# Optimization experiments

Measured on AMD Instinct MI355X. Metric: run time of the kernel, lower is better.

The kernel has to match this reference:

```python
import jax, jax.numpy as jnp
import numpy as np

SPARSE_COMPRESSION_RATIO = 0.5  # config.sparse_compression_ratio


def setup_inputs() -> dict:
    key = jax.random.key(0)
    kv_cache = jax.random.normal(key, (2, 32, 4096, 128), dtype=jnp.float32)
    return {"kv_cache": kv_cache}


def reference(kv_cache):
    # elements_to_keep = int(numel * (1 - ratio))
    total = kv_cache.size
    k = int(total * (1.0 - SPARSE_COMPRESSION_RATIO))
    flat = kv_cache.reshape(-1)
    # torch.topk(|x|, k, largest=True) -> indices of k largest magnitudes
    _, top_idx = jax.lax.top_k(jnp.abs(flat), k)
    # scatter mask, then elementwise multiply (zeros out non-top-k entries)
    mask = jnp.zeros((total,), dtype=jnp.bool_).at[top_idx].set(True)
    return kv_cache * mask.reshape(kv_cache.shape)
```

## Files before the change

kernel.cpp:

```cpp
#include <hip/hip_runtime.h>
#include <stdint.h>


#define NTHR 256
#define MASK31 0x7fffffffu

#define SH_OFF    0
#define SH_BINS   8192
#define CH_OFF    8192
#define CH_BINS   4096
#define SCL_OFF   12288
#define L3_OFF    12304
#define L3_CAP    4096
#define PAIRS_OFF (L3_OFF + 2 * L3_CAP)
#define PAIRS_CAP (1u << 20)
#define ZERO_WORDS (SCL_OFF + 16)

#define STG_CAP   2048

__global__ void zero_ws_kernel(uint32_t* __restrict__ ws) {
    int i = blockIdx.x * blockDim.x + threadIdx.x;
    if (i < ZERO_WORDS) ws[i] = 0;
}

__global__ void sample_hist_kernel(const uint4* __restrict__ xv, long long n4,
                                   uint32_t* __restrict__ ws) {
    __shared__ uint32_t lh[SH_BINS];
    for (int i = threadIdx.x; i < SH_BINS; i += NTHR) lh[i] = 0;
    __syncthreads();
    long long S4 = n4 >> 5;
    long long T = (long long)gridDim.x * NTHR;
    for (long long s = (long long)blockIdx.x * NTHR + threadIdx.x; s < S4; s += T) {
        long long g = s >> 6;
        long long idx4 = g * 2048 + ((g & 31) << 6) + (s & 63);
        uint4 v = xv[idx4];
        atomicAdd(&lh[(v.x & MASK31) >> 18], 1u);
        atomicAdd(&lh[(v.y & MASK31) >> 18], 1u);
        atomicAdd(&lh[(v.z & MASK31) >> 18], 1u);
        atomicAdd(&lh[(v.w & MASK31) >> 18], 1u);
    }
    __syncthreads();
    for (int i = threadIdx.x; i < SH_BINS; i += NTHR)
        if (lh[i]) atomicAdd(&ws[SH_OFF + i], lh[i]);
}

__global__ void sel_bracket_kernel(uint32_t* __restrict__ ws,
                                   uint32_t ksmM, uint32_t kspM) {
    __shared__ uint32_t lh[SH_BINS];
    __shared__ uint32_t csum[NTHR];
    __shared__ uint32_t cpre[NTHR];
    __shared__ int sBHi, sB1;
    for (int i = threadIdx.x; i < SH_BINS; i += NTHR) lh[i] = ws[SH_OFF + i];
    if (threadIdx.x == 0) { sBHi = -1; sB1 = -1; }
    __syncthreads();
    uint32_t s = 0;
    for (int i = 0; i < 32; ++i) s += lh[threadIdx.x * 32 + i];
    csum[threadIdx.x] = s;
    __syncthreads();
    if (threadIdx.x == 0) {
        uint32_t run = 0;
        for (int c = NTHR - 1; c >= 0; --c) { cpre[c] = run; run += csum[c]; }
    }
    __syncthreads();
    {
        int c = threadIdx.x;
        int hitHi = -1, hitB1 = -1;
        uint32_t excl = cpre[c];
        for (int bb = c * 32 + 31; bb >= c * 32; --bb) {
            uint32_t cnt = lh[bb];
            uint32_t incl = excl + cnt;
            if (hitHi < 0 && incl >= ksmM) hitHi = bb;
            if (hitB1 < 0 && excl >= kspM) hitB1 = bb;
            excl = incl;
        }
        if (hitHi >= 0) atomicMax(&sBHi, hitHi);
        if (hitB1 >= 0) atomicMax(&sB1, hitB1);
    }
    __syncthreads();
    if (threadIdx.x == 0) {
        int bHi = sBHi < 0 ? 0 : sBHi;
        int bLo = sB1 + 1;
        if (bLo > bHi) bLo = bHi;
        if (bLo < 0) bLo = 0;
        int sbins = bHi - bLo + 1;
        int clog = 0; while ((1 << clog) < sbins) ++clog;
        int spanBits = 18 + clog;
        int shift1 = spanBits - 12;
        if (shift1 < 0) shift1 = 0;
        ws[SCL_OFF + 0] = ((uint32_t)bLo) << 18;
        ws[SCL_OFF + 1] = ((uint32_t)(bHi + 1)) << 18;
        ws[SCL_OFF + 2] = (uint32_t)shift1;
    }
}

__global__ void fused_main_kernel(const uint32_t* __restrict__ x,
                                  uint32_t* __restrict__ out, long long n,
                                  uint32_t* __restrict__ ws) {
    __shared__ uint2 stage[STG_CAP];
    __shared__ uint32_t cnt, sBase, redHi[NTHR / 64];
    const uint32_t uLo = ws[SCL_OFF + 0];
    const uint32_t uHi = ws[SCL_OFF + 1];
    const uint32_t span = uHi - uLo;
    if (threadIdx.x == 0) cnt = 0u;
    __syncthreads();

    const uint4* __restrict__ xv = (const uint4*)x;
    uint4* __restrict__ ov = (uint4*)out;
    uint2* __restrict__ gpairs = (uint2*)(ws + PAIRS_OFF);
    long long n4 = n >> 2;
    const long long stride = (long long)gridDim.x * NTHR;
    const long long i0 = (long long)blockIdx.x * NTHR + threadIdx.x;

    uint32_t myHi = 0;
    uint32_t hitIter = 0;
    uint32_t it = 0;
    long long i = i0;
    for (; i + stride < n4; i += 2 * stride, it += 2) {
        uint4 va = xv[i];
        uint4 vb = xv[i + stride];
        uint32_t a0 = va.x & MASK31, a1 = va.y & MASK31;
        uint32_t a2 = va.z & MASK31, a3 = va.w & MASK31;
        uint32_t b0 = vb.x & MASK31, b1 = vb.y & MASK31;
        uint32_t b2 = vb.z & MASK31, b3 = vb.w & MASK31;
        myHi += (uint32_t)(a0 >= uHi) + (uint32_t)(a1 >= uHi)
              + (uint32_t)(a2 >= uHi) + (uint32_t)(a3 >= uHi)
              + (uint32_t)(b0 >= uHi) + (uint32_t)(b1 >= uHi)
              + (uint32_t)(b2 >= uHi) + (uint32_t)(b3 >= uHi);
        uint32_t ha = (uint32_t)((a0 - uLo) < span) | (uint32_t)((a1 - uLo) < span)
                    | (uint32_t)((a2 - uLo) < span) | (uint32_t)((a3 - uLo) < span);
        uint32_t hb = (uint32_t)((b0 - uLo) < span) | (uint32_t)((b1 - uLo) < span)
                    | (uint32_t)((b2 - uLo) < span) | (uint32_t)((b3 - uLo) < span);
        hitIter |= ha << (it & 31);
        hitIter |= hb << ((it + 1) & 31);
        uint4 oa, ob;
        oa.x = (a0 >= uHi) ? va.x : 0u;
        oa.y = (a1 >= uHi) ? va.y : 0u;
        oa.z = (a2 >= uHi) ? va.z : 0u;
        oa.w = (a3 >= uHi) ? va.w : 0u;
        ob.x = (b0 >= uHi) ? vb.x : 0u;
        ob.y = (b1 >= uHi) ? vb.y : 0u;
        ob.z = (b2 >= uHi) ? vb.z : 0u;
        ob.w = (b3 >= uHi) ? vb.w : 0u;
        ov[i] = oa;
        ov[i + stride] = ob;
    }
    if (i < n4) {
        uint4 v = xv[i];
        uint32_t a0 = v.x & MASK31, a1 = v.y & MASK31;
        uint32_t a2 = v.z & MASK31, a3 = v.w & MASK31;
        myHi += (uint32_t)(a0 >= uHi) + (uint32_t)(a1 >= uHi)
              + (uint32_t)(a2 >= uHi) + (uint32_t)(a3 >= uHi);
        uint32_t ha = (uint32_t)((a0 - uLo) < span) | (uint32_t)((a1 - uLo) < span)
                    | (uint32_t)((a2 - uLo) < span) | (uint32_t)((a3 - uLo) < span);
        hitIter |= ha << (it & 31);
        uint4 o;
        o.x = (a0 >= uHi) ? v.x : 0u;
        o.y = (a1 >= uHi) ? v.y : 0u;
        o.z = (a2 >= uHi) ? v.z : 0u;
        o.w = (a3 >= uHi) ? v.w : 0u;
        ov[i] = o;
    }

#define PUSHP(val, eidx) { \
    uint32_t p_ = atomicAdd(&cnt, 1u); \
    uint2 pr_ = make_uint2((val), (eidx)); \
    if (p_ < STG_CAP) stage[p_] = pr_; \
    else { uint32_t g_ = atomicAdd(&ws[SCL_OFF + 4], 1u); \
           if (g_ < PAIRS_CAP) gpairs[g_] = pr_; } }

    if (blockIdx.x == 0) {
        for (long long idx = (n4 << 2) + threadIdx.x; idx < n; idx += NTHR) {
            uint32_t v = x[idx];
            uint32_t u = v & MASK31;
            myHi += (uint32_t)(u >= uHi);
            if (u - uLo < span) PUSHP(v, (uint32_t)idx)
            out[idx] = (u >= uHi) ? v : 0u;
        }
    }

    while (hitIter) {
        uint32_t b = __ffs(hitIter) - 1u;
        hitIter &= hitIter - 1u;
        for (long long ii = i0 + (long long)b * stride; ii < n4; ii += (stride << 5)) {
            uint4 v = xv[ii];
            uint32_t e0 = (uint32_t)(ii << 2);
            uint32_t u;
            u = v.x & MASK31; if (u - uLo < span) PUSHP(v.x, e0 + 0u)
            u = v.y & MASK31; if (u - uLo < span) PUSHP(v.y, e0 + 1u)
            u = v.z & MASK31; if (u - uLo < span) PUSHP(v.z, e0 + 2u)
            u = v.w & MASK31; if (u - uLo < span) PUSHP(v.w, e0 + 3u)
        }
    }
#undef PUSHP

    for (int o = 32; o > 0; o >>= 1) myHi += __shfl_down(myHi, o);
    if ((threadIdx.x & 63) == 0) redHi[threadIdx.x >> 6] = myHi;
    __syncthreads();
    if (threadIdx.x == 0) {
        uint32_t tot = 0;
        for (int w = 0; w < NTHR / 64; ++w) tot += redHi[w];
        if (tot) atomicAdd(&ws[SCL_OFF + 3], tot);
        uint32_t c = cnt < STG_CAP ? cnt : STG_CAP;
        cnt = c;
        sBase = atomicAdd(&ws[SCL_OFF + 4], c);
    }
    __syncthreads();
    uint32_t c = cnt, bw = sBase;
    for (uint32_t q = threadIdx.x; q < c; q += NTHR)
        if (bw + q < PAIRS_CAP) gpairs[bw + q] = stage[q];
}

__global__ void cand_hist_kernel(uint32_t* __restrict__ ws) {
    __shared__ uint32_t lh[CH_BINS];
    uint32_t G = ws[SCL_OFF + 4]; if (G > PAIRS_CAP) G = PAIRS_CAP;
    uint32_t uLo = ws[SCL_OFF + 0], shift1 = ws[SCL_OFF + 2];
    for (int i = threadIdx.x; i < CH_BINS; i += NTHR) lh[i] = 0;
    __syncthreads();
    const uint2* pairs = (const uint2*)(ws + PAIRS_OFF);
    uint32_t stride = gridDim.x * NTHR;
    for (uint32_t i = blockIdx.x * NTHR + threadIdx.x; i < G; i += stride) {
        uint32_t u = pairs[i].x & MASK31;
        atomicAdd(&lh[((u - uLo) >> shift1) & (CH_BINS - 1)], 1u);
    }
    __syncthreads();
    for (int i = threadIdx.x; i < CH_BINS; i += NTHR)
        if (lh[i]) atomicAdd(&ws[CH_OFF + i], lh[i]);
}

__global__ void sel_gather_kernel(uint32_t* __restrict__ ws, uint32_t k) {
    __shared__ uint32_t lh[CH_BINS];
    __shared__ uint32_t csum[NTHR];
    __shared__ uint32_t cpre[NTHR];
    __shared__ uint32_t sBase2, sRem2, sKp;
    for (int i = threadIdx.x; i < CH_BINS; i += NTHR) lh[i] = ws[CH_OFF + i];
    __syncthreads();
    uint32_t s = 0;
    for (int i = 0; i < 16; ++i) s += lh[threadIdx.x * 16 + i];
    csum[threadIdx.x] = s;
    __syncthreads();
    if (threadIdx.x == 0) {
        uint32_t run = 0;
        for (int c = NTHR - 1; c >= 0; --c) { cpre[c] = run; run += csum[c]; }
        uint32_t cntHi = ws[SCL_OFF + 3];
        uint32_t total = cpre[0] + csum[0];
        uint32_t kp = (k > cntHi) ? (k - cntHi) : 1u;
        if (kp > total) kp = total;
        if (kp < 1u) kp = 1u;
        sKp = kp;
    }
    __syncthreads();
    uint32_t kp = sKp;
    if (cpre[threadIdx.x] < kp && kp <= cpre[threadIdx.x] + csum[threadIdx.x]) {
        uint32_t excl = cpre[threadIdx.x];
        for (int bb = threadIdx.x * 16 + 15; bb >= threadIdx.x * 16; --bb) {
            uint32_t cnt = lh[bb];
            if (excl + cnt >= kp) {
                sBase2 = ws[SCL_OFF + 0] + (((uint32_t)bb) << ws[SCL_OFF + 2]);
                sRem2 = kp - excl;
                break;
            }
            excl += cnt;
        }
    }
    __syncthreads();
    if (threadIdx.x == 0) { ws[SCL_OFF + 5] = sBase2; ws[SCL_OFF + 6] = sRem2; }
    uint32_t base2 = sBase2;
    uint32_t width = 1u << ws[SCL_OFF + 2];
    uint32_t G = ws[SCL_OFF + 4]; if (G > PAIRS_CAP) G = PAIRS_CAP;
    const uint2* pairs = (const uint2*)(ws + PAIRS_OFF);
    uint2* l3 = (uint2*)(ws + L3_OFF);
    uint32_t stride = gridDim.x * NTHR;
    for (uint32_t i = blockIdx.x * NTHR + threadIdx.x; i < G; i += stride) {
        uint2 pr = pairs[i];
        uint32_t u = pr.x & MASK31;
        if (u - base2 < width) {
            uint32_t p = atomicAdd(&ws[SCL_OFF + 7], 1u);
            if (p < L3_CAP) l3[p] = pr;
        }
    }
}

__global__ void final_fixup_kernel(uint32_t* __restrict__ ws,
                                   uint32_t* __restrict__ out) {
    __shared__ uint2 l3s[L3_CAP];
    uint32_t c3 = ws[SCL_OFF + 7]; if (c3 > L3_CAP) c3 = L3_CAP;
    uint32_t base2 = ws[SCL_OFF + 5], rem2 = ws[SCL_OFF + 6];
    uint32_t width = 1u << ws[SCL_OFF + 2];
    uint32_t tHi2 = base2 + width;
    const uint2* l3 = (const uint2*)(ws + L3_OFF);
    for (uint32_t q = threadIdx.x; q < c3; q += NTHR) l3s[q] = l3[q];
    __syncthreads();
    uint32_t G = ws[SCL_OFF + 4]; if (G > PAIRS_CAP) G = PAIRS_CAP;
    const uint2* pairs = (const uint2*)(ws + PAIRS_OFF);
    uint32_t stride = gridDim.x * NTHR;
    for (uint32_t i = blockIdx.x * NTHR + threadIdx.x; i < G; i += stride) {
        uint2 pr = pairs[i];
        uint32_t u = pr.x & MASK31;
        if (u >= tHi2) {
            out[pr.y] = pr.x;
        } else if (u - base2 < width) {
            uint32_t rank = 0;
            for (uint32_t p = 0; p < c3; ++p) {
                uint2 q2 = l3s[p];
                uint32_t up = q2.x & MASK31;
                rank += (up > u || (up == u && q2.y < pr.y)) ? 1u : 0u;
            }
            if (rank < rem2) out[pr.y] = pr.x;
        }
    }
}

extern "C" void kernel_launch(void* const* d_in, const int* in_sizes, int n_in,
                              void* d_out, int out_size, void* d_ws, size_t ws_size,
                              hipStream_t stream) {
    const uint32_t* x = (const uint32_t*)d_in[0];
    uint32_t* out = (uint32_t*)d_out;
    uint32_t* ws = (uint32_t*)d_ws;
    long long n = (long long)in_sizes[0];

    const double ratio = 0.5;
    long long k = (long long)((double)n * (1.0 - ratio));
    if (k < 1) k = 1;
    if (k > n) k = n;

    long long n4 = n >> 2;
    long long S = (n4 >> 5) << 2;
    long long ks = (long long)((double)k * ((double)S / (double)n));
    const long long M = 4500;
    uint32_t ksmM = (uint32_t)((ks - M) < 1 ? 1 : (ks - M));
    uint32_t kspM = (uint32_t)((ks + M) > S ? S : (ks + M));

    long long nBlk = (n4 + (long long)NTHR * 16 - 1) / ((long long)NTHR * 16);
    if (nBlk < 1) nBlk = 1;
    if (nBlk > 8192) nBlk = 8192;
    int grid = (int)nBlk;

    zero_ws_kernel<<<(ZERO_WORDS + NTHR - 1) / NTHR, NTHR, 0, stream>>>(ws);
    sample_hist_kernel<<<512, NTHR, 0, stream>>>((const uint4*)x, n4, ws);
    sel_bracket_kernel<<<1, NTHR, 0, stream>>>(ws, ksmM, kspM);
    fused_main_kernel<<<grid, NTHR, 0, stream>>>(x, out, n, ws);
    cand_hist_kernel<<<256, NTHR, 0, stream>>>(ws);
    sel_gather_kernel<<<256, NTHR, 0, stream>>>(ws, (uint32_t)k);
    final_fixup_kernel<<<256, NTHR, 0, stream>>>(ws, out);
}
```

Before: 153.1 us.

## Unroll main pass with nontemporal stores and sample contiguous histogram chunks

The main classify-and-mask pass now handles four strided vectors per iteration instead of two. It writes its output with nontemporal stores and declares launch bounds, aiming to keep more loads in flight and to stop the output from filling the cache. The sampling histogram now reads 8 contiguous 256-vector runs per block across 128 evenly spaced chunks, replacing the strided gather over 512 blocks, with the sample size in the host code adjusted to match. This relies on contiguous chunks being representative of the data, which holds for random inputs but could widen the selected bracket on structured data.

```diff
diff --git a/kernel.cpp b/kernel.cpp
--- a/kernel.cpp
+++ b/kernel.cpp
@@ -4,6 +4,8 @@
 
 #define NTHR 256
 #define MASK31 0x7fffffffu
+
+typedef unsigned int v4u __attribute__((ext_vector_type(4)));
 
 #define SH_OFF    0
 #define SH_BINS   8192
@@ -28,16 +30,17 @@
     __shared__ uint32_t lh[SH_BINS];
     for (int i = threadIdx.x; i < SH_BINS; i += NTHR) lh[i] = 0;
     __syncthreads();
-    long long S4 = n4 >> 5;
-    long long T = (long long)gridDim.x * NTHR;
-    for (long long s = (long long)blockIdx.x * NTHR + threadIdx.x; s < S4; s += T) {
-        long long g = s >> 6;
-        long long idx4 = g * 2048 + ((g & 31) << 6) + (s & 63);
-        uint4 v = xv[idx4];
-        atomicAdd(&lh[(v.x & MASK31) >> 18], 1u);
-        atomicAdd(&lh[(v.y & MASK31) >> 18], 1u);
-        atomicAdd(&lh[(v.z & MASK31) >> 18], 1u);
-        atomicAdd(&lh[(v.w & MASK31) >> 18], 1u);
+    long long chunkStride = n4 >> 7;
+    long long base = (long long)blockIdx.x * chunkStride + threadIdx.x;
+    for (int j = 0; j < 8; ++j) {
+        long long idx = base + (long long)j * NTHR;
+        if (idx < n4) {
+            uint4 v = xv[idx];
+            atomicAdd(&lh[(v.x & MASK31) >> 18], 1u);
+            atomicAdd(&lh[(v.y & MASK31) >> 18], 1u);
+            atomicAdd(&lh[(v.z & MASK31) >> 18], 1u);
+            atomicAdd(&lh[(v.w & MASK31) >> 18], 1u);
+        }
     }
     __syncthreads();
     for (int i = threadIdx.x; i < SH_BINS; i += NTHR)
@@ -93,9 +96,10 @@
     }
 }
 
-__global__ void fused_main_kernel(const uint32_t* __restrict__ x,
-                                  uint32_t* __restrict__ out, long long n,
-                                  uint32_t* __restrict__ ws) {
+__global__ __launch_bounds__(NTHR, 4)
+void fused_main_kernel(const uint32_t* __restrict__ x,
+                       uint32_t* __restrict__ out, long long n,
+                       uint32_t* __restrict__ ws) {
     __shared__ uint2 stage[STG_CAP];
     __shared__ uint32_t cnt, sBase, redHi[NTHR / 64];
     const uint32_t uLo = ws[SCL_OFF + 0];
@@ -104,62 +108,53 @@
     if (threadIdx.x == 0) cnt = 0u;
     __syncthreads();
 
-    const uint4* __restrict__ xv = (const uint4*)x;
-    uint4* __restrict__ ov = (uint4*)out;
+    const v4u* __restrict__ xv = (const v4u*)x;
+    v4u* __restrict__ ov = (v4u*)out;
     uint2* __restrict__ gpairs = (uint2*)(ws + PAIRS_OFF);
     long long n4 = n >> 2;
     const long long stride = (long long)gridDim.x * NTHR;
     const long long i0 = (long long)blockIdx.x * NTHR + threadIdx.x;
 
     uint32_t myHi = 0;
-    uint32_t hitIter = 0;
+    uint32_t hitMask = 0;
     uint32_t it = 0;
     long long i = i0;
-    for (; i + stride < n4; i += 2 * stride, it += 2) {
-        uint4 va = xv[i];
-        uint4 vb = xv[i + stride];
-        uint32_t a0 = va.x & MASK31, a1 = va.y & MASK31;
-        uint32_t a2 = va.z & MASK31, a3 = va.w & MASK31;
-        uint32_t b0 = vb.x & MASK31, b1 = vb.y & MASK31;
-        uint32_t b2 = vb.z & MASK31, b3 = vb.w & MASK31;
-        myHi += (uint32_t)(a0 >= uHi) + (uint32_t)(a1 >= uHi)
-              + (uint32_t)(a2 >= uHi) + (uint32_t)(a3 >= uHi)
-              + (uint32_t)(b0 >= uHi) + (uint32_t)(b1 >= uHi)
-              + (uint32_t)(b2 >= uHi) + (uint32_t)(b3 >= uHi);
-        uint32_t ha = (uint32_t)((a0 - uLo) < span) | (uint32_t)((a1 - uLo) < span)
-                    | (uint32_t)((a2 - uLo) < span) | (uint32_t)((a3 - uLo) < span);
-        uint32_t hb = (uint32_t)((b0 - uLo) < span) | (uint32_t)((b1 - uLo) < span)
-                    | (uint32_t)((b2 - uLo) < span) | (uint32_t)((b3 - uLo) < span);
-        hitIter |= ha << (it & 31);
-        hitIter |= hb << ((it + 1) & 31);
-        uint4 oa, ob;
-        oa.x = (a0 >= uHi) ? va.x : 0u;
-        oa.y = (a1 >= uHi) ? va.y : 0u;
-        oa.z = (a2 >= uHi) ? va.z : 0u;
-        oa.w = (a3 >= uHi) ? va.w : 0u;
-        ob.x = (b0 >= uHi) ? vb.x : 0u;
-        ob.y = (b1 >= uHi) ? vb.y : 0u;
-        ob.z = (b2 >= uHi) ? vb.z : 0u;
-        ob.w = (b3 >= uHi) ? vb.w : 0u;
-        ov[i] = oa;
-        ov[i + stride] = ob;
-    }
-    if (i < n4) {
-        uint4 v = xv[i];
-        uint32_t a0 = v.x & MASK31, a1 = v.y & MASK31;
-        uint32_t a2 = v.z & MASK31, a3 = v.w & MASK31;
-        myHi += (uint32_t)(a0 >= uHi) + (uint32_t)(a1 >= uHi)
-              + (uint32_t)(a2 >= uHi) + (uint32_t)(a3 >= uHi);
-        uint32_t ha = (uint32_t)((a0 - uLo) < span) | (uint32_t)((a1 - uLo) < span)
-                    | (uint32_t)((a2 - uLo) < span) | (uint32_t)((a3 - uLo) < span);
-        hitIter |= ha << (it & 31);
-        uint4 o;
-        o.x = (a0 >= uHi) ? v.x : 0u;
-        o.y = (a1 >= uHi) ? v.y : 0u;
-        o.z = (a2 >= uHi) ? v.z : 0u;
-        o.w = (a3 >= uHi) ? v.w : 0u;
-        ov[i] = o;
-    }
+
+#define CLASS(v, o, hb) { \
+    uint32_t c0 = v.x & MASK31, c1 = v.y & MASK31, c2 = v.z & MASK31, c3 = v.w & MASK31; \
+    myHi += (uint32_t)(c0 >= uHi) + (uint32_t)(c1 >= uHi) \
+          + (uint32_t)(c2 >= uHi) + (uint32_t)(c3 >= uHi); \
+    o.x = (c0 >= uHi) ? v.x : 0u; o.y = (c1 >= uHi) ? v.y : 0u; \
+    o.z = (c2 >= uHi) ? v.z : 0u; o.w = (c3 >= uHi) ? v.w : 0u; \
+    hb = (uint32_t)((c0 - uLo) < span) | (uint32_t)((c1 - uLo) < span) \
+       | (uint32_t)((c2 - uLo) < span) | (uint32_t)((c3 - uLo) < span); }
+
+    for (; i + 3 * stride < n4; i += 4 * stride, it += 4) {
+        v4u v0 = xv[i];
+        v4u v1 = xv[i + stride];
+        v4u v2 = xv[i + 2 * stride];
+        v4u v3 = xv[i + 3 * stride];
+        v4u o0, o1, o2, o3;
+        uint32_t h0, h1, h2, h3;
+        CLASS(v0, o0, h0) CLASS(v1, o1, h1) CLASS(v2, o2, h2) CLASS(v3, o3, h3)
+        hitMask |= h0 << (it & 31);
+        hitMask |= h1 << ((it + 1) & 31);
+        hitMask |= h2 << ((it + 2) & 31);
+        hitMask |= h3 << ((it + 3) & 31);
+        __builtin_nontemporal_store(o0, &ov[i]);
+        __builtin_nontemporal_store(o1, &ov[i + stride]);
+        __builtin_nontemporal_store(o2, &ov[i + 2 * stride]);
+        __builtin_nontemporal_store(o3, &ov[i + 3 * stride]);
+    }
+    for (; i < n4; i += stride, ++it) {
+        v4u v = xv[i];
+        v4u o;
+        uint32_t hb;
+        CLASS(v, o, hb)
+        hitMask |= hb << (it & 31);
+        __builtin_nontemporal_store(o, &ov[i]);
+    }
+#undef CLASS
 
 #define PUSHP(val, eidx) { \
     uint32_t p_ = atomicAdd(&cnt, 1u); \
@@ -178,11 +173,11 @@
         }
     }
 
-    while (hitIter) {
-        uint32_t b = __ffs(hitIter) - 1u;
-        hitIter &= hitIter - 1u;
+    while (hitMask) {
+        uint32_t b = __ffs(hitMask) - 1u;
+        hitMask &= hitMask - 1u;
         for (long long ii = i0 + (long long)b * stride; ii < n4; ii += (stride << 5)) {
-            uint4 v = xv[ii];
+            v4u v = xv[ii];
             uint32_t e0 = (uint32_t)(ii << 2);
             uint32_t u;
             u = v.x & MASK31; if (u - uLo < span) PUSHP(v.x, e0 + 0u)
@@ -324,7 +319,8 @@
     if (k > n) k = n;
 
     long long n4 = n >> 2;
-    long long S = (n4 >> 5) << 2;
+    long long S = ((n4 >> 7) >= 2048) ? (128LL * NTHR * 8 * 4)
+                                      : (n4 << 2);
     long long ks = (long long)((double)k * ((double)S / (double)n));
     const long long M = 4500;
     uint32_t ksmM = (uint32_t)((ks - M) < 1 ? 1 : (ks - M));
@@ -336,7 +332,7 @@
     int grid = (int)nBlk;
 
     zero_ws_kernel<<<(ZERO_WORDS + NTHR - 1) / NTHR, NTHR, 0, stream>>>(ws);
-    sample_hist_kernel<<<512, NTHR, 0, stream>>>((const uint4*)x, n4, ws);
+    sample_hist_kernel<<<128, NTHR, 0, stream>>>((const uint4*)x, n4, ws);
     sel_bracket_kernel<<<1, NTHR, 0, stream>>>(ws, ksmM, kspM);
     fused_main_kernel<<<grid, NTHR, 0, stream>>>(x, out, n, ws);
     cand_hist_kernel<<<256, NTHR, 0, stream>>>(ws);
```

Result: faster. 143.2 us (-6.5%).
